# Performance work log

Measured on AMD Instinct MI355X. Metric: run time of the kernel, lower is better.

## Reference

```python
import jax, jax.numpy as jnp
import numpy as np

NUM_CLASSES = 100000
FEAT_DIM = 512
BATCH = 256
CLAMP_MIN = 1e-12
CLAMP_MAX = 1e12


def setup_inputs() -> dict:
    key = jax.random.key(0)
    k_x, k_lbl, k_c = jax.random.split(key, 3)
    x = jax.random.normal(k_x, (BATCH, FEAT_DIM), dtype=jnp.float32)
    label = jax.random.randint(k_lbl, (BATCH,), 0, NUM_CLASSES, dtype=jnp.int64)
    # xavier_uniform_ on (num_classes, feat_dim): bound = sqrt(6/(fan_in+fan_out))
    bound = float(np.sqrt(6.0 / (NUM_CLASSES + FEAT_DIM)))
    centers = jax.random.uniform(k_c, (NUM_CLASSES, FEAT_DIM), dtype=jnp.float32,
                                 minval=-bound, maxval=bound)
    return {"x": x, "label": label, "centers": centers}


def reference(x, label, centers):
    # Original: full [B, C] squared-distance matrix, then per-row gather of the
    # entry at the true label, clamp, mean. Equivalent fused form: gather the
    # label's center and take the squared L2 distance directly.
    c = centers[label]                        # [B, D] gather
    diff = x - c
    dist = jnp.sum(diff * diff, axis=1)       # [B] = dis[i, label[i]]
    dist = jnp.clip(dist, CLAMP_MIN, CLAMP_MAX)
    return jnp.mean(dist)
```

## Files before the change

kernel.cpp:

```cpp
#include <hip/hip_runtime.h>

#define CL_BATCH 256
#define CL_FEAT  512
#define CL_CLAMP_MIN 1e-12f
#define CL_CLAMP_MAX 1e12f

__global__ __launch_bounds__(64) void center_loss_rows(
    const float* __restrict__ x,
    const int* __restrict__ label,
    const float* __restrict__ centers,
    float* __restrict__ row_dist)
{
    const int b = blockIdx.x;
    const int t = threadIdx.x;

    const int lbl = label[b];

    const float4* __restrict__ xr =
        reinterpret_cast<const float4*>(x + (size_t)b * CL_FEAT);
    const float4* __restrict__ cr =
        reinterpret_cast<const float4*>(centers + (size_t)lbl * CL_FEAT);

    float4 xv0 = xr[t];
    float4 cv0 = cr[t];
    float4 xv1 = xr[t + 64];
    float4 cv1 = cr[t + 64];

    float s = 0.0f;
    float d;
    d = xv0.x - cv0.x; s = fmaf(d, d, s);
    d = xv0.y - cv0.y; s = fmaf(d, d, s);
    d = xv0.z - cv0.z; s = fmaf(d, d, s);
    d = xv0.w - cv0.w; s = fmaf(d, d, s);
    d = xv1.x - cv1.x; s = fmaf(d, d, s);
    d = xv1.y - cv1.y; s = fmaf(d, d, s);
    d = xv1.z - cv1.z; s = fmaf(d, d, s);
    d = xv1.w - cv1.w; s = fmaf(d, d, s);

    #pragma unroll
    for (int off = 32; off > 0; off >>= 1)
        s += __shfl_down(s, off, 64);

    if (t == 0) {
        s = fminf(fmaxf(s, CL_CLAMP_MIN), CL_CLAMP_MAX);
        row_dist[b] = s;
    }
}

__global__ __launch_bounds__(64) void center_loss_reduce(
    const float* __restrict__ row_dist,
    float* __restrict__ out)
{
    const int t = threadIdx.x;
    const float4* __restrict__ r = reinterpret_cast<const float4*>(row_dist);
    float4 v = r[t];
    float s = (v.x + v.y) + (v.z + v.w);

    #pragma unroll
    for (int off = 32; off > 0; off >>= 1)
        s += __shfl_down(s, off, 64);

    if (t == 0)
        out[0] = s * (1.0f / (float)CL_BATCH);
}

extern "C" void kernel_launch(void* const* d_in, const int* in_sizes, int n_in,
                              void* d_out, int out_size, void* d_ws, size_t ws_size,
                              hipStream_t stream)
{
    const float* x       = (const float*)d_in[0];
    const int*   label   = (const int*)d_in[1];
    const float* centers = (const float*)d_in[2];
    float* out = (float*)d_out;
    float* row_dist = (float*)d_ws;

    center_loss_rows<<<CL_BATCH, 64, 0, stream>>>(x, label, centers, row_dist);
    center_loss_reduce<<<1, 64, 0, stream>>>(row_dist, out);
}
```

Baseline: 11.54 us.

## Fuse row distance and final reduction into one cooperative kernel with grid sync

Merges the two launches into a single cooperative kernel. Each 256-thread block handles four rows, reduces them in LDS and publishes one partial with a release store. A grid-wide sync then lets block 0 sum the 64 partials. This removes the second kernel launch and its launch gap. The cost is cooperative-launch overhead and a grid barrier, which may be as expensive as the launch it replaces.

```diff
diff --git a/kernel.cpp b/kernel.cpp
--- a/kernel.cpp
+++ b/kernel.cpp
@@ -1,33 +1,41 @@
 #include <hip/hip_runtime.h>
+#include <hip/hip_cooperative_groups.h>
 
-#define CL_BATCH 256
-#define CL_FEAT  512
+namespace cg = cooperative_groups;
+
+#define CL_BATCH   256
+#define CL_FEAT    512
+#define CL_BLOCKS  64
+#define CL_THREADS 256
+#define CL_ROWS_PER_BLOCK (CL_BATCH / CL_BLOCKS)
 #define CL_CLAMP_MIN 1e-12f
 #define CL_CLAMP_MAX 1e12f
 
-__global__ __launch_bounds__(64) void center_loss_rows(
+__global__ __launch_bounds__(CL_THREADS) void center_loss_fused(
     const float* __restrict__ x,
-    const int* __restrict__ label,
+    const int*   __restrict__ label,
     const float* __restrict__ centers,
-    float* __restrict__ row_dist)
+    float*       __restrict__ partials,
+    float*       __restrict__ out)
 {
-    const int b = blockIdx.x;
-    const int t = threadIdx.x;
+    const int wid  = threadIdx.x >> 6;
+    const int lane = threadIdx.x & 63;
+    const int b    = blockIdx.x * CL_ROWS_PER_BLOCK + wid;
+
+    __shared__ float lds[CL_ROWS_PER_BLOCK];
 
     const int lbl = label[b];
-
     const float4* __restrict__ xr =
         reinterpret_cast<const float4*>(x + (size_t)b * CL_FEAT);
     const float4* __restrict__ cr =
         reinterpret_cast<const float4*>(centers + (size_t)lbl * CL_FEAT);
 
-    float4 xv0 = xr[t];
-    float4 cv0 = cr[t];
-    float4 xv1 = xr[t + 64];
-    float4 cv1 = cr[t + 64];
+    float4 xv0 = xr[lane];
+    float4 cv0 = cr[lane];
+    float4 xv1 = xr[lane + 64];
+    float4 cv1 = cr[lane + 64];
 
-    float s = 0.0f;
-    float d;
+    float s = 0.0f, d;
     d = xv0.x - cv0.x; s = fmaf(d, d, s);
     d = xv0.y - cv0.y; s = fmaf(d, d, s);
     d = xv0.z - cv0.z; s = fmaf(d, d, s);
@@ -41,27 +49,29 @@
     for (int off = 32; off > 0; off >>= 1)
         s += __shfl_down(s, off, 64);
 
-    if (t == 0) {
+    if (lane == 0) {
         s = fminf(fmaxf(s, CL_CLAMP_MIN), CL_CLAMP_MAX);
-        row_dist[b] = s;
+        lds[wid] = s;
     }
-}
+    __syncthreads();
 
-__global__ __launch_bounds__(64) void center_loss_reduce(
-    const float* __restrict__ row_dist,
-    float* __restrict__ out)
-{
-    const int t = threadIdx.x;
-    const float4* __restrict__ r = reinterpret_cast<const float4*>(row_dist);
-    float4 v = r[t];
-    float s = (v.x + v.y) + (v.z + v.w);
+    if (threadIdx.x == 0) {
+        float p = (lds[0] + lds[1]) + (lds[2] + lds[3]);
+        __hip_atomic_store(&partials[blockIdx.x], p,
+                           __ATOMIC_RELEASE, __HIP_MEMORY_SCOPE_AGENT);
+    }
 
-    #pragma unroll
-    for (int off = 32; off > 0; off >>= 1)
-        s += __shfl_down(s, off, 64);
+    cg::this_grid().sync();
 
-    if (t == 0)
-        out[0] = s * (1.0f / (float)CL_BATCH);
+    if (blockIdx.x == 0 && wid == 0) {
+        float v = __hip_atomic_load(&partials[lane],
+                                    __ATOMIC_ACQUIRE, __HIP_MEMORY_SCOPE_AGENT);
+        #pragma unroll
+        for (int off = 32; off > 0; off >>= 1)
+            v += __shfl_down(v, off, 64);
+        if (lane == 0)
+            out[0] = v * (1.0f / (float)CL_BATCH);
+    }
 }
 
 extern "C" void kernel_launch(void* const* d_in, const int* in_sizes, int n_in,
@@ -71,9 +81,12 @@
     const float* x       = (const float*)d_in[0];
     const int*   label   = (const int*)d_in[1];
     const float* centers = (const float*)d_in[2];
-    float* out = (float*)d_out;
-    float* row_dist = (float*)d_ws;
+    float* out      = (float*)d_out;
+    float* partials = (float*)d_ws;
 
-    center_loss_rows<<<CL_BATCH, 64, 0, stream>>>(x, label, centers, row_dist);
-    center_loss_reduce<<<1, 64, 0, stream>>>(row_dist, out);
+    void* args[] = { (void*)&x, (void*)&label, (void*)&centers,
+                     (void*)&partials, (void*)&out };
+    hipLaunchCooperativeKernel((const void*)center_loss_fused,
+                               dim3(CL_BLOCKS), dim3(CL_THREADS),
+                               args, 0, stream);
 }
```

Result: slower. 33.55 us (+190.7%).
